# Performance work log

Measured on AMD Instinct MI355X. Metric: run time of the kernel, lower is better.

The kernel has to match this reference:

```python
import jax, jax.numpy as jnp
import numpy as np

N = 50000
E = 800000
DES, TW, NUMP, CATP = 768, 768, 4, 3
EMB = 384
THIRD = EMB // 3  # 128


def _lin(key, fan_in, fan_out):
    k1, k2 = jax.random.split(key)
    bound = 1.0 / np.sqrt(fan_in)
    W = jax.random.uniform(k1, (fan_in, fan_out), jnp.float32, -bound, bound)
    b = jax.random.uniform(k2, (fan_out,), jnp.float32, -bound, bound)
    return W, b


def setup_inputs() -> dict:
    key = jax.random.key(0)
    ks = jax.random.split(key, 16)
    des = jax.random.normal(ks[0], (N, DES), jnp.float32)
    tweet = jax.random.normal(ks[1], (N, TW), jnp.float32)
    num_prop = jax.random.normal(ks[2], (N, NUMP), jnp.float32)
    cat_prop = jax.random.normal(ks[3], (N, CATP), jnp.float32)
    edge_index = jax.random.randint(ks[4], (2, E), 0, N, jnp.int64)
    W_des, b_des = _lin(ks[5], DES, THIRD)
    W_num, b_num = _lin(ks[6], NUMP, THIRD)
    W_cat, b_cat = _lin(ks[7], CATP, THIRD)
    W_in, b_in = _lin(ks[8], EMB, EMB)
    W_g1, b_g1 = _lin(ks[9], EMB, EMB)
    W_g2, b_g2 = _lin(ks[10], EMB, EMB)
    W_o1, b_o1 = _lin(ks[11], EMB, EMB)
    W_o2, b_o2 = _lin(ks[12], EMB, 2)
    return dict(des=des, tweet=tweet, num_prop=num_prop, cat_prop=cat_prop,
                edge_index=edge_index,
                W_des=W_des, b_des=b_des, W_num=W_num, b_num=b_num,
                W_cat=W_cat, b_cat=b_cat, W_in=W_in, b_in=b_in,
                W_g1=W_g1, b_g1=b_g1, W_g2=W_g2, b_g2=b_g2,
                W_o1=W_o1, b_o1=b_o1, W_o2=W_o2, b_o2=b_o2)


def _leaky(x):
    return jax.nn.leaky_relu(x, 0.01)


def _gcn_conv(x, edge_index, W, b):
    # PyG GCNConv: x' = D^{-1/2} (A + I) D^{-1/2} (x W) + b
    src, dst = edge_index[0], edge_index[1]
    x = x @ W  # [N, out]
    n = x.shape[0]
    deg = jax.ops.segment_sum(jnp.ones(src.shape[0], x.dtype), dst, num_segments=n) + 1.0  # self-loop
    dinv = jax.lax.rsqrt(deg)  # deg >= 1
    norm = dinv[src] * dinv[dst]  # [E]
    msg = x[src] * norm[:, None]  # [E, out] gather
    agg = jax.ops.segment_sum(msg, dst, num_segments=n)  # scatter-add
    agg = agg + x * (dinv * dinv)[:, None]  # self-loop contribution
    return agg + b


def reference(des, tweet, num_prop, cat_prop, edge_index,
              W_des, b_des, W_num, b_num, W_cat, b_cat, W_in, b_in,
              W_g1, b_g1, W_g2, b_g2, W_o1, b_o1, W_o2, b_o2):
    # eval mode: dropout is identity
    d = _leaky(des @ W_des + b_des)
    n = _leaky(num_prop @ W_num + b_num)
    c = _leaky(cat_prop @ W_cat + b_cat)
    x = jnp.concatenate((d, n, c), axis=1)  # [N, EMB]
    x = _leaky(x @ W_in + b_in)
    x = _gcn_conv(x, edge_index, W_g1, b_g1)
    x = _gcn_conv(x, edge_index, W_g2, b_g2)
    x = _leaky(x @ W_o1 + b_o1)
    return x @ W_o2 + b_o2  # [N, 2]
```

## Files before the change

### kernel.cpp

```cpp
#include <hip/hip_runtime.h>
#include <hip/hip_bf16.h>
#include <cstdint>

#define NFEAT 384
#define DESK 768
#define THIRD 128

typedef __bf16 bf16x8 __attribute__((ext_vector_type(8)));
typedef unsigned short u16x8 __attribute__((ext_vector_type(8)));
typedef unsigned short u16x4 __attribute__((ext_vector_type(4)));
typedef float f32x16 __attribute__((ext_vector_type(16)));
typedef _Float16 h16x2 __attribute__((ext_vector_type(2)));

__device__ __forceinline__ float leaky(float x) { return x > 0.f ? x : 0.01f * x; }

__device__ __forceinline__ unsigned short bfhi(float x) {
  unsigned int u = __float_as_uint(x);
  u += 0x7fffu + ((u >> 16) & 1u);
  return (unsigned short)(u >> 16);
}
__device__ __forceinline__ float bf2f(unsigned short h) {
  return __uint_as_float(((unsigned int)h) << 16);
}
__device__ __forceinline__ void bsplit(float x, unsigned short& h,
                                       unsigned short& l) {
  h = bfhi(x);
  l = bfhi(x - bf2f(h));
}

__device__ __forceinline__ int swz(int kb, int row, int ROWS) {
  return (kb * ROWS + (row ^ (kb << 1))) * 8;
}

#define MFMA(a, b, c) __builtin_amdgcn_mfma_f32_32x32x16_bf16(a, b, c, 0, 0, 0)

template <int AFP32, int EPI, int BM, int DBUF>
__global__ __launch_bounds__(256, 2) void mfma_gemm(
    const float* __restrict__ Af, const unsigned short* __restrict__ Ahi,
    const unsigned short* __restrict__ Alo,
    const unsigned short* __restrict__ BThi,
    const unsigned short* __restrict__ BTlo, _Float16* __restrict__ Ch16,
    unsigned short* __restrict__ Chi, unsigned short* __restrict__ Clo,
    const float* __restrict__ bias, int M, int K, int ldc) {
  __shared__ unsigned short AhiL[DBUF + 1][4 * BM * 8];
  __shared__ unsigned short AloL[DBUF + 1][4 * BM * 8];
  __shared__ unsigned short BhiL[DBUF + 1][4 * 128 * 8];
  __shared__ unsigned short BloL[DBUF + 1][4 * 128 * 8];
  const int tid = threadIdx.x;
  const int lane = tid & 63;
  const int w = tid >> 6;
  constexpr int MR = BM / 64;
  const int wm = (w >> 1) * (BM / 2);
  const int wn = (w & 1) * 64;
  const int lm = lane & 31, lk = lane >> 5;

  int bx = blockIdx.x, by = blockIdx.y;
  if (gridDim.y == 3) {
    int lin = by * gridDim.x + bx;
    int ng = gridDim.x >> 3;
    int full = ng * 24;
    if (lin < full) {
      int g = lin / 24, x = lin - g * 24;
      bx = g * 8 + (x & 7);
      by = x >> 3;
    } else {
      int rem = lin - full;
      int mrem = gridDim.x - (ng << 3);
      bx = (ng << 3) + rem % mrem;
      by = rem / mrem;
    }
  }
  const int m_base = bx * BM, n_base = by * 128;

  f32x16 acc[MR][2];
#pragma unroll
  for (int mi = 0; mi < MR; mi++)
#pragma unroll
    for (int nt = 0; nt < 2; nt++)
#pragma unroll
      for (int r = 0; r < 16; r++) acc[mi][nt][r] = 0.f;

  constexpr int AIT_F = BM / 32;
  constexpr int AIT_H = BM / 64;
  float4 pa[3][AIT_F];
  u16x8 pah[3][AIT_H], pal[3][AIT_H];
  u16x8 pbh[3][2], pbl[3][2];

  auto loadA = [&](int kt, int s) {
    if (AFP32) {
#pragma unroll
      for (int it = 0; it < AIT_F; it++) {
        int r = (tid >> 3) + it * 32;
        int gr = m_base + r;
        float4 av = make_float4(0.f, 0.f, 0.f, 0.f);
        if (gr < M) av = *(const float4*)&Af[(size_t)gr * K + kt + (tid & 7) * 4];
        pa[s][it] = av;
      }
    } else {
#pragma unroll
      for (int it = 0; it < AIT_H; it++) {
        int r = (tid >> 2) + it * 64;
        int gr = m_base + r;
        u16x8 vh = {0, 0, 0, 0, 0, 0, 0, 0};
        u16x8 vl = {0, 0, 0, 0, 0, 0, 0, 0};
        if (gr < M) {
          vh = *(const u16x8*)&Ahi[(size_t)gr * K + kt + (tid & 3) * 8];
          vl = *(const u16x8*)&Alo[(size_t)gr * K + kt + (tid & 3) * 8];
        }
        pah[s][it] = vh;
        pal[s][it] = vl;
      }
    }
  };
  auto loadB = [&](int kt, int s) {
#pragma unroll
    for (int it = 0; it < 2; it++) {
      int n = (tid >> 2) + it * 64;
      pbh[s][it] = *(const u16x8*)&BThi[(size_t)(n_base + n) * K + kt + (tid & 3) * 8];
      pbl[s][it] = *(const u16x8*)&BTlo[(size_t)(n_base + n) * K + kt + (tid & 3) * 8];
    }
  };
  auto storeLDS = [&](int s, int b) {
    if (AFP32) {
#pragma unroll
      for (int it = 0; it < AIT_F; it++) {
        int r = (tid >> 3) + it * 32;
        int q = tid & 7;
        float4 av = pa[s][it];
        unsigned short h0, h1, h2, h3, l0, l1, l2, l3;
        bsplit(av.x, h0, l0);
        bsplit(av.y, h1, l1);
        bsplit(av.z, h2, l2);
        bsplit(av.w, h3, l3);
        int base = swz(q >> 1, r, BM) + (q & 1) * 4;
        u16x4 th;
        th.x = h0; th.y = h1; th.z = h2; th.w = h3;
        u16x4 tl;
        tl.x = l0; tl.y = l1; tl.z = l2; tl.w = l3;
        *(u16x4*)&AhiL[b][base] = th;
        *(u16x4*)&AloL[b][base] = tl;
      }
    } else {
#pragma unroll
      for (int it = 0; it < AIT_H; it++) {
        int r = (tid >> 2) + it * 64;
        int kb = tid & 3;
        *(u16x8*)&AhiL[b][swz(kb, r, BM)] = pah[s][it];
        *(u16x8*)&AloL[b][swz(kb, r, BM)] = pal[s][it];
      }
    }
#pragma unroll
    for (int it = 0; it < 2; it++) {
      int n = (tid >> 2) + it * 64;
      int kb = tid & 3;
      *(u16x8*)&BhiL[b][swz(kb, n, 128)] = pbh[s][it];
      *(u16x8*)&BloL[b][swz(kb, n, 128)] = pbl[s][it];
    }
  };
  auto compute = [&](int b) {
#pragma unroll
    for (int ks = 0; ks < 2; ks++) {
      int kb = 2 * ks + lk;
      bf16x8 ah[MR], al[MR];
#pragma unroll
      for (int mi = 0; mi < MR; mi++) {
        ah[mi] = __builtin_bit_cast(
            bf16x8, *(const u16x8*)&AhiL[b][swz(kb, wm + mi * 32 + lm, BM)]);
        al[mi] = __builtin_bit_cast(
            bf16x8, *(const u16x8*)&AloL[b][swz(kb, wm + mi * 32 + lm, BM)]);
      }
      bf16x8 bh0 = __builtin_bit_cast(
          bf16x8, *(const u16x8*)&BhiL[b][swz(kb, wn + lm, 128)]);
      bf16x8 bh1 = __builtin_bit_cast(
          bf16x8, *(const u16x8*)&BhiL[b][swz(kb, wn + 32 + lm, 128)]);
      bf16x8 bl0 = __builtin_bit_cast(
          bf16x8, *(const u16x8*)&BloL[b][swz(kb, wn + lm, 128)]);
      bf16x8 bl1 = __builtin_bit_cast(
          bf16x8, *(const u16x8*)&BloL[b][swz(kb, wn + 32 + lm, 128)]);
#pragma unroll
      for (int mi = 0; mi < MR; mi++) {
        acc[mi][0] = MFMA(ah[mi], bh0, acc[mi][0]);
        acc[mi][1] = MFMA(ah[mi], bh1, acc[mi][1]);
        acc[mi][0] = MFMA(ah[mi], bl0, acc[mi][0]);
        acc[mi][1] = MFMA(ah[mi], bl1, acc[mi][1]);
        acc[mi][0] = MFMA(al[mi], bh0, acc[mi][0]);
        acc[mi][1] = MFMA(al[mi], bh1, acc[mi][1]);
      }
    }
  };

  const int NK = K >> 5;
  loadA(0, 0);
  loadB(0, 0);
  loadA(32, 1);
  loadB(32, 1);
  loadA(64, 2);
  loadB(64, 2);

  if (DBUF) {
    storeLDS(0, 0);
    __syncthreads();
    for (int m6 = 0; m6 < NK / 6; m6++) {
#pragma unroll
      for (int ph = 0; ph < 6; ph++) {
        const int i = m6 * 6 + ph;
        if (i + 1 < NK) storeLDS((ph + 1) % 3, (ph + 1) & 1);
        if (i + 3 < NK) {
          loadA((i + 3) << 5, ph % 3);
          loadB((i + 3) << 5, ph % 3);
        }
        compute(ph & 1);
        __syncthreads();
      }
    }
  } else {
    for (int m3 = 0; m3 < NK / 3; m3++) {
#pragma unroll
      for (int ph = 0; ph < 3; ph++) {
        const int i = m3 * 3 + ph;
        storeLDS(ph, 0);
        __syncthreads();
        if (i + 3 < NK) {
          loadA((i + 3) << 5, ph);
          loadB((i + 3) << 5, ph);
        }
        compute(0);
        __syncthreads();
      }
    }
  }

  const int colb = n_base + wn;
#pragma unroll
  for (int mi = 0; mi < MR; mi++) {
#pragma unroll
    for (int nt = 0; nt < 2; nt++) {
      f32x16 v = acc[mi][nt];
      int col = colb + nt * 32 + lm;
      float bv = (EPI == 0) ? bias[col] : 0.f;
      int rb = m_base + wm + mi * 32 + 4 * lk;
      int p = col / 48;
      size_t pbase = (size_t)p * M * 48 + (col - p * 48);
#pragma unroll
      for (int rg = 0; rg < 16; rg++) {
        int row = rb + (rg & 3) + 8 * (rg >> 2);
        if (row < M) {
          float x = v[rg];
          if (EPI == 0) {
            x = leaky(x + bv);
            unsigned short h, l;
            bsplit(x, h, l);
            Chi[(size_t)row * ldc + col] = h;
            Clo[(size_t)row * ldc + col] = l;
          } else {
            Ch16[pbase + (size_t)row * 48] = (_Float16)x;
          }
        }
      }
    }
  }
}

__global__ __launch_bounds__(256) void split_transpose_b(
    const float* __restrict__ s0, unsigned short* __restrict__ h0,
    unsigned short* __restrict__ l0, const float* __restrict__ s1,
    unsigned short* __restrict__ h1, unsigned short* __restrict__ l1,
    const float* __restrict__ s2, unsigned short* __restrict__ h2,
    unsigned short* __restrict__ l2) {
  int z = blockIdx.z;
  const float* src = z == 0 ? s0 : (z == 1 ? s1 : s2);
  unsigned short* dsthi = z == 0 ? h0 : (z == 1 ? h1 : h2);
  unsigned short* dstlo = z == 0 ? l0 : (z == 1 ? l1 : l2);
  int R = z == 0 ? 768 : 384;
  int C = z == 0 ? 128 : 384;
  int c0 = blockIdx.x * 32, r0 = blockIdx.y * 32;
  if (c0 >= C || r0 >= R) return;
  __shared__ float tile[32][33];
  int tx = threadIdx.x & 31, ty = threadIdx.x >> 5;
#pragma unroll
  for (int i = 0; i < 4; i++)
    tile[ty + i * 8][tx] = src[(size_t)(r0 + ty + i * 8) * C + c0 + tx];
  __syncthreads();
#pragma unroll
  for (int i = 0; i < 4; i++) {
    int c = c0 + ty + i * 8, r = r0 + tx;
    float v = tile[tx][ty + i * 8];
    unsigned short h, l;
    bsplit(v, h, l);
    dsthi[(size_t)c * R + r] = h;
    dstlo[(size_t)c * R + r] = l;
  }
}

__global__ __launch_bounds__(256) void gemm384(const float* __restrict__ A,
                                               const float* __restrict__ B,
                                               float* __restrict__ C) {
  __shared__ float As[16][68];
  __shared__ float Bs[16][64];
  const int tid = threadIdx.x;
  const int mb = blockIdx.x * 64;
  const int nb = blockIdx.y * 64;
  float acc[4][4] = {};
  const int arow = tid >> 2, akq = tid & 3;
  const int brow = tid >> 4, bc4 = tid & 15;
  const int m0 = (tid >> 4) * 4, n0 = (tid & 15) * 4;
  for (int kk = 0; kk < 384; kk += 16) {
    float4 av = *(const float4*)&A[(mb + arow) * 384 + kk + akq * 4];
    As[akq * 4 + 0][arow] = av.x;
    As[akq * 4 + 1][arow] = av.y;
    As[akq * 4 + 2][arow] = av.z;
    As[akq * 4 + 3][arow] = av.w;
    *(float4*)&Bs[brow][bc4 * 4] =
        *(const float4*)&B[(kk + brow) * 384 + nb + bc4 * 4];
    __syncthreads();
#pragma unroll
    for (int k = 0; k < 16; k++) {
      float4 a4 = *(const float4*)&As[k][m0];
      float4 b4 = *(const float4*)&Bs[k][n0];
      float a[4] = {a4.x, a4.y, a4.z, a4.w};
      float b[4] = {b4.x, b4.y, b4.z, b4.w};
#pragma unroll
      for (int i = 0; i < 4; i++)
#pragma unroll
        for (int j = 0; j < 4; j++) acc[i][j] = fmaf(a[i], b[j], acc[i][j]);
    }
    __syncthreads();
  }
#pragma unroll
  for (int i = 0; i < 4; i++)
#pragma unroll
    for (int j = 0; j < 4; j++)
      C[(mb + m0 + i) * 384 + nb + n0 + j] = acc[i][j];
}

__global__ void uv_kernel(const float* __restrict__ T1,
                          const float* __restrict__ W_o1,
                          const float* __restrict__ b_g1,
                          const float* __restrict__ b_g2,
                          const float* __restrict__ b_o1, float* __restrict__ u,
                          float* __restrict__ v) {
  int j = blockIdx.x * blockDim.x + threadIdx.x;
  if (j < 384) {
    float su = 0.f, sv = 0.f;
    for (int k = 0; k < 384; k++) {
      su = fmaf(T1[k * 384 + j], b_g1[k], su);
      sv = fmaf(W_o1[k * 384 + j], b_g2[k], sv);
    }
    u[j] = su;
    v[j] = sv + b_o1[j];
  }
}

__global__ __launch_bounds__(256) void numcat_kernel(
    const float* __restrict__ num, const float* __restrict__ cat,
    const float* __restrict__ Wn, const float* __restrict__ bn,
    const float* __restrict__ Wc, const float* __restrict__ bc,
    unsigned short* __restrict__ x0hi, unsigned short* __restrict__ x0lo,
    int N) {
  int c = threadIdx.x;
  for (int i = blockIdx.x; i < N; i += gridDim.x) {
    float val;
    if (c < 128) {
      val = bn[c];
      val = fmaf(num[i * 4 + 0], Wn[0 * 128 + c], val);
      val = fmaf(num[i * 4 + 1], Wn[1 * 128 + c], val);
      val = fmaf(num[i * 4 + 2], Wn[2 * 128 + c], val);
      val = fmaf(num[i * 4 + 3], Wn[3 * 128 + c], val);
    } else {
      int cc = c - 128;
      val = bc[cc];
      val = fmaf(cat[i * 3 + 0], Wc[0 * 128 + cc], val);
      val = fmaf(cat[i * 3 + 1], Wc[1 * 128 + cc], val);
      val = fmaf(cat[i * 3 + 2], Wc[2 * 128 + cc], val);
    }
    val = leaky(val);
    unsigned short h, l;
    bsplit(val, h, l);
    size_t o = (size_t)i * NFEAT + 128 + c;
    x0hi[o] = h;
    x0lo[o] = l;
  }
}

__global__ void count_kernel(const int* __restrict__ dst, int* __restrict__ deg,
                             int E) {
  int e = blockIdx.x * blockDim.x + threadIdx.x;
  if (e < E) atomicAdd(&deg[dst[e]], 1);
}

__global__ void scan_reduce(const int* __restrict__ deg,
                            int* __restrict__ partial, int N) {
  __shared__ int sm[512];
  int i = blockIdx.x * 512 + threadIdx.x;
  sm[threadIdx.x] = (i < N) ? deg[i] : 0;
  __syncthreads();
  for (int off = 256; off; off >>= 1) {
    if (threadIdx.x < off) sm[threadIdx.x] += sm[threadIdx.x + off];
    __syncthreads();
  }
  if (threadIdx.x == 0) partial[blockIdx.x] = sm[0];
}

__global__ void scan_top(int* partial, int nb) {
  if (threadIdx.x == 0 && blockIdx.x == 0) {
    int run = 0;
    for (int b = 0; b < nb; b++) {
      int t = partial[b];
      partial[b] = run;
      run += t;
    }
  }
}

__global__ void scan_down(const int* __restrict__ deg,
                          const int* __restrict__ partial,
                          int* __restrict__ offsets, int* __restrict__ cursor,
                          float* __restrict__ dinv, int N, int E) {
  __shared__ int sm[512];
  int t = threadIdx.x;
  int i = blockIdx.x * 512 + t;
  int val = (i < N) ? deg[i] : 0;
  sm[t] = val;
  __syncthreads();
  for (int off = 1; off < 512; off <<= 1) {
    int add = (t >= off) ? sm[t - off] : 0;
    __syncthreads();
    sm[t] += add;
    __syncthreads();
  }
  if (i < N) {
    int ex = partial[blockIdx.x] + sm[t] - val;
    offsets[i] = ex;
    cursor[i] = ex;
    dinv[i] = 1.0f / sqrtf((float)val + 1.0f);
  }
  if (i == 0) offsets[N] = E;
}

__global__ void fill_kernel(const int* __restrict__ src,
                            const int* __restrict__ dst,
                            int* __restrict__ cursor,
                            int* __restrict__ csr_off,
                            float* __restrict__ csr_w,
                            const float* __restrict__ dinv, int E) {
  int e = blockIdx.x * blockDim.x + threadIdx.x;
  if (e < E) {
    int s = src[e], d = dst[e];
    int slot = atomicAdd(&cursor[d], 1);
    csr_off[slot] = s * 48;
    csr_w[slot] = dinv[s] * dinv[d];
  }
}

__global__ void init_out(const float* __restrict__ b_o2,
                         float* __restrict__ out, int N) {
  int i = blockIdx.x * blockDim.x + threadIdx.x;
  if (i < N) {
    out[2 * i + 0] = b_o2[0];
    out[2 * i + 1] = b_o2[1];
  }
}

template <int WRITE_S, int FINAL>
__global__ __launch_bounds__(192) void agg_slice(
    const _Float16* __restrict__ xin, _Float16* __restrict__ xout,
    const int* __restrict__ offsets, const int* __restrict__ csr_off,
    const float* __restrict__ csr_w, const float* __restrict__ dinv,
    float* __restrict__ sout, const float* __restrict__ svec,
    const float* __restrict__ uvec, const float* __restrict__ vvec,
    const float* __restrict__ W_o2, float* __restrict__ out, int N) {
  const int t = threadIdx.x;
  const int team = t / 24;
  const int l = t - team * 24;
  const int slice = blockIdx.x & 7;
  const int sb = blockIdx.x >> 3;
  const int teams_per_slice = (gridDim.x >> 3) * 8;
  const _Float16* xp = xin + (size_t)slice * N * 48;
  const int t0 = sb * 8 + team;
  __shared__ float red[192][2];

  float u0 = 0.f, u1 = 0.f, vc0 = 0.f, vc1 = 0.f;
  float w00 = 0.f, w01 = 0.f, w10 = 0.f, w11 = 0.f;
  if (FINAL) {
    const int f = slice * 48 + 2 * l;
    u0 = uvec[f];
    u1 = uvec[f + 1];
    vc0 = vvec[f];
    vc1 = vvec[f + 1];
    w00 = W_o2[f * 2 + 0];
    w01 = W_o2[f * 2 + 1];
    w10 = W_o2[(f + 1) * 2 + 0];
    w11 = W_o2[(f + 1) * 2 + 1];
  }

  auto dorow = [&](int i, float& ax, float& ay, float& wsum) {
    int beg = offsets[i], end = offsets[i + 1];
    float di = dinv[i];
    float dii = di * di;
    h16x2 xs = *(const h16x2*)&xp[(size_t)i * 48 + 2 * l];
    float A0x = dii * (float)xs.x, A0y = dii * (float)xs.y;
    float A1x = 0.f, A1y = 0.f, A2x = 0.f, A2y = 0.f, A3x = 0.f, A3y = 0.f;
    wsum = dii;
    int j = beg;
    for (; j + 8 <= end; j += 8) {
      int o0 = csr_off[j + 0], o1 = csr_off[j + 1], o2 = csr_off[j + 2],
          o3 = csr_off[j + 3];
      int o4 = csr_off[j + 4], o5 = csr_off[j + 5], o6 = csr_off[j + 6],
          o7 = csr_off[j + 7];
      float w0 = csr_w[j + 0], w1 = csr_w[j + 1], w2 = csr_w[j + 2],
            w3 = csr_w[j + 3];
      float w4 = csr_w[j + 4], w5 = csr_w[j + 5], w6 = csr_w[j + 6],
            w7 = csr_w[j + 7];
      h16x2 v0 = *(const h16x2*)&xp[o0 + 2 * l];
      h16x2 v1 = *(const h16x2*)&xp[o1 + 2 * l];
      h16x2 v2 = *(const h16x2*)&xp[o2 + 2 * l];
      h16x2 v3 = *(const h16x2*)&xp[o3 + 2 * l];
      h16x2 v4 = *(const h16x2*)&xp[o4 + 2 * l];
      h16x2 v5 = *(const h16x2*)&xp[o5 + 2 * l];
      h16x2 v6 = *(const h16x2*)&xp[o6 + 2 * l];
      h16x2 v7 = *(const h16x2*)&xp[o7 + 2 * l];
      A0x = fmaf(w0, (float)v0.x, A0x);
      A0y = fmaf(w0, (float)v0.y, A0y);
      A1x = fmaf(w1, (float)v1.x, A1x);
      A1y = fmaf(w1, (float)v1.y, A1y);
      A2x = fmaf(w2, (float)v2.x, A2x);
      A2y = fmaf(w2, (float)v2.y, A2y);
      A3x = fmaf(w3, (float)v3.x, A3x);
      A3y = fmaf(w3, (float)v3.y, A3y);
      A0x = fmaf(w4, (float)v4.x, A0x);
      A0y = fmaf(w4, (float)v4.y, A0y);
      A1x = fmaf(w5, (float)v5.x, A1x);
      A1y = fmaf(w5, (float)v5.y, A1y);
      A2x = fmaf(w6, (float)v6.x, A2x);
      A2y = fmaf(w6, (float)v6.y, A2y);
      A3x = fmaf(w7, (float)v7.x, A3x);
      A3y = fmaf(w7, (float)v7.y, A3y);
      if (WRITE_S) wsum += ((w0 + w1) + (w2 + w3)) + ((w4 + w5) + (w6 + w7));
    }
    for (; j < end; j++) {
      float wj = csr_w[j];
      h16x2 vj = *(const h16x2*)&xp[csr_off[j] + 2 * l];
      A0x = fmaf(wj, (float)vj.x, A0x);
      A0y = fmaf(wj, (float)vj.y, A0y);
      if (WRITE_S) wsum += wj;
    }
    ax = (A0x + A1x) + (A2x + A3x);
    ay = (A0y + A1y) + (A2y + A3y);
  };

  if (FINAL) {
    const int iters = (N + teams_per_slice - 1) / teams_per_slice;
    for (int it = 0; it < iters; it++) {
      const int i = t0 + it * teams_per_slice;
      float c0 = 0.f, c1 = 0.f;
      if (i < N) {
        float ax, ay, wsum;
        dorow(i, ax, ay, wsum);
        float si = svec[i];
        float q0 = leaky(ax + si * u0 + vc0);
        float q1 = leaky(ay + si * u1 + vc1);
        c0 = q0 * w00 + q1 * w10;
        c1 = q0 * w01 + q1 * w11;
      }
      red[t][0] = c0;
      red[t][1] = c1;
      __syncthreads();
      if (t < 16) {
        int tm = t >> 1, c = t & 1;
        int i2 = sb * 8 + tm + it * teams_per_slice;
        if (i2 < N) {
          float s = 0.f;
#pragma unroll
          for (int k = 0; k < 24; k++) s += red[tm * 24 + k][c];
          atomicAdd(&out[i2 * 2 + c], s);
        }
      }
      __syncthreads();
    }
  } else {
    _Float16* op = xout + (size_t)slice * N * 48;
    for (int i = t0; i < N; i += teams_per_slice) {
      float ax, ay, wsum;
      dorow(i, ax, ay, wsum);
      h16x2 r;
      r.x = (_Float16)ax;
      r.y = (_Float16)ay;
      *(h16x2*)&op[(size_t)i * 48 + 2 * l] = r;
      if (WRITE_S && slice == 0 && l == 0) sout[i] = wsum;
    }
  }
}

extern "C" void kernel_launch(void* const* d_in, const int* in_sizes, int n_in,
                              void* d_out, int out_size, void* d_ws,
                              size_t ws_size, hipStream_t stream) {
  const float* des = (const float*)d_in[0];
  const float* num_prop = (const float*)d_in[2];
  const float* cat_prop = (const float*)d_in[3];
  const int* edge = (const int*)d_in[4];
  const float* W_des = (const float*)d_in[5];
  const float* b_des = (const float*)d_in[6];
  const float* W_num = (const float*)d_in[7];
  const float* b_num = (const float*)d_in[8];
  const float* W_cat = (const float*)d_in[9];
  const float* b_cat = (const float*)d_in[10];
  const float* W_in = (const float*)d_in[11];
  const float* b_in = (const float*)d_in[12];
  const float* W_g1 = (const float*)d_in[13];
  const float* b_g1 = (const float*)d_in[14];
  const float* W_g2 = (const float*)d_in[15];
  const float* b_g2 = (const float*)d_in[16];
  const float* W_o1 = (const float*)d_in[17];
  const float* b_o1 = (const float*)d_in[18];
  const float* W_o2 = (const float*)d_in[19];
  const float* b_o2 = (const float*)d_in[20];
  float* out = (float*)d_out;

  const int N = in_sizes[0] / DESK;
  const int E = in_sizes[4] / 2;
  const int* esrc = edge;
  const int* edst = edge + E;

  char* ws = (char*)d_ws;
  size_t off = 0;
  auto alloc = [&](size_t n) {
    off = (off + 255) & ~(size_t)255;
    size_t o = off;
    off += n;
    return o;
  };
  float* bufA = (float*)(ws + alloc((size_t)N * NFEAT * 4));
  float* bufB = (float*)(ws + alloc((size_t)N * NFEAT * 4));
  int* deg = (int*)(ws + alloc((size_t)N * 4));
  int* offsets = (int*)(ws + alloc((size_t)(N + 1) * 4));
  int* cursor = (int*)(ws + alloc((size_t)N * 4));
  int* partial = (int*)(ws + alloc(1024 * 4));
  float* dinv = (float*)(ws + alloc((size_t)N * 4));
  float* svec = (float*)(ws + alloc((size_t)N * 4));
  int* csr_off = (int*)(ws + alloc((size_t)E * 4));
  float* csr_w = (float*)(ws + alloc((size_t)E * 4));
  float* T1 = (float*)(ws + alloc(384 * 384 * 4));
  float* Mmat = (float*)(ws + alloc(384 * 384 * 4));
  float* uvec = (float*)(ws + alloc(384 * 4));
  float* vvec = (float*)(ws + alloc(384 * 4));
  unsigned short* WdThi = (unsigned short*)(ws + alloc(768 * 128 * 2));
  unsigned short* WdTlo = (unsigned short*)(ws + alloc(768 * 128 * 2));
  unsigned short* WiThi = (unsigned short*)(ws + alloc(384 * 384 * 2));
  unsigned short* WiTlo = (unsigned short*)(ws + alloc(384 * 384 * 2));
  unsigned short* MmThi = (unsigned short*)(ws + alloc(384 * 384 * 2));
  unsigned short* MmTlo = (unsigned short*)(ws + alloc(384 * 384 * 2));
  (void)ws_size;
  (void)n_in;
  (void)out_size;

  unsigned short* x0hi = (unsigned short*)bufA;
  unsigned short* x0lo = x0hi + (size_t)N * NFEAT;
  unsigned short* x1hi = (unsigned short*)bufB;
  unsigned short* x1lo = x1hi + (size_t)N * NFEAT;
  _Float16* yb = (_Float16*)bufA;
  _Float16* w1 = (_Float16*)bufB;

  hipMemsetAsync(deg, 0, (size_t)N * 4, stream);

  dim3 g6(6, 6);
  gemm384<<<g6, 256, 0, stream>>>(W_g2, W_o1, T1);
  gemm384<<<g6, 256, 0, stream>>>(W_g1, T1, Mmat);
  uv_kernel<<<2, 256, 0, stream>>>(T1, W_o1, b_g1, b_g2, b_o1, uvec, vvec);
  split_transpose_b<<<dim3(12, 24, 3), 256, 0, stream>>>(
      W_des, WdThi, WdTlo, W_in, WiThi, WiTlo, Mmat, MmThi, MmTlo);

  const int MT = (N + 127) / 128;
  const int MT64 = (N + 63) / 64;
  mfma_gemm<1, 0, 64, 0><<<dim3(MT64, 1), 256, 0, stream>>>(
      des, nullptr, nullptr, WdThi, WdTlo, nullptr, x0hi, x0lo, b_des, N, DESK,
      NFEAT);
  numcat_kernel<<<1024, 256, 0, stream>>>(num_prop, cat_prop, W_num, b_num,
                                          W_cat, b_cat, x0hi, x0lo, N);
  mfma_gemm<0, 0, 128, 1><<<dim3(MT, 3), 256, 0, stream>>>(
      nullptr, x0hi, x0lo, WiThi, WiTlo, nullptr, x1hi, x1lo, b_in, N, NFEAT,
      NFEAT);
  mfma_gemm<0, 1, 128, 1><<<dim3(MT, 3), 256, 0, stream>>>(
      nullptr, x1hi, x1lo, MmThi, MmTlo, yb, nullptr, nullptr, nullptr, N,
      NFEAT, NFEAT);

  const int EB = (E + 255) / 256;
  count_kernel<<<EB, 256, 0, stream>>>(edst, deg, E);
  const int NB = (N + 511) / 512;
  scan_reduce<<<NB, 512, 0, stream>>>(deg, partial, N);
  scan_top<<<1, 64, 0, stream>>>(partial, NB);
  scan_down<<<NB, 512, 0, stream>>>(deg, partial, offsets, cursor, dinv, N, E);
  fill_kernel<<<EB, 256, 0, stream>>>(esrc, edst, cursor, csr_off, csr_w, dinv,
                                      E);
  init_out<<<(N + 255) / 256, 256, 0, stream>>>(b_o2, out, N);

  const int NBS = 512;
  agg_slice<1, 0><<<8 * NBS, 192, 0, stream>>>(
      yb, w1, offsets, csr_off, csr_w, dinv, svec, nullptr, nullptr, nullptr,
      nullptr, nullptr, N);
  agg_slice<0, 1><<<8 * NBS, 192, 0, stream>>>(
      w1, nullptr, offsets, csr_off, csr_w, dinv, nullptr, svec, uvec, vvec,
      W_o2, out, N);
}
```

Measured before the change: 1.023 ms.

## Parallelize GCN aggregation across edges within a block instead of rows per team

Result: slower. 1.453 ms (+42.1%).

```diff
diff --git a/kernel.cpp b/kernel.cpp
--- a/kernel.cpp
+++ b/kernel.cpp
@@ -462,7 +462,7 @@
 }
 
 template <int WRITE_S, int FINAL>
-__global__ __launch_bounds__(192) void agg_slice(
+__global__ __launch_bounds__(192) void agg_ep(
     const _Float16* __restrict__ xin, _Float16* __restrict__ xout,
     const int* __restrict__ offsets, const int* __restrict__ csr_off,
     const float* __restrict__ csr_w, const float* __restrict__ dinv,
@@ -470,19 +470,23 @@
     const float* __restrict__ uvec, const float* __restrict__ vvec,
     const float* __restrict__ W_o2, float* __restrict__ out, int N) {
   const int t = threadIdx.x;
-  const int team = t / 24;
-  const int l = t - team * 24;
+  const int e8 = t / 24;
+  const int l = t - e8 * 24;
   const int slice = blockIdx.x & 7;
   const int sb = blockIdx.x >> 3;
-  const int teams_per_slice = (gridDim.x >> 3) * 8;
+  const int nsb = gridDim.x >> 3;
   const _Float16* xp = xin + (size_t)slice * N * 48;
-  const int t0 = sb * 8 + team;
-  __shared__ float red[192][2];
+  _Float16* op = FINAL ? nullptr : xout + (size_t)slice * N * 48;
+  __shared__ int ssrc[64];
+  __shared__ float sw[64];
+  __shared__ float red[8][24][2];
+  __shared__ float rw[8];
+  __shared__ float rc[24][2];
 
   float u0 = 0.f, u1 = 0.f, vc0 = 0.f, vc1 = 0.f;
   float w00 = 0.f, w01 = 0.f, w10 = 0.f, w11 = 0.f;
-  if (FINAL) {
-    const int f = slice * 48 + 2 * l;
+  if (FINAL && t < 24) {
+    const int f = slice * 48 + 2 * t;
     u0 = uvec[f];
     u1 = uvec[f + 1];
     vc0 = vvec[f];
@@ -493,100 +497,74 @@
     w11 = W_o2[(f + 1) * 2 + 1];
   }
 
-  auto dorow = [&](int i, float& ax, float& ay, float& wsum) {
-    int beg = offsets[i], end = offsets[i + 1];
-    float di = dinv[i];
-    float dii = di * di;
-    h16x2 xs = *(const h16x2*)&xp[(size_t)i * 48 + 2 * l];
-    float A0x = dii * (float)xs.x, A0y = dii * (float)xs.y;
-    float A1x = 0.f, A1y = 0.f, A2x = 0.f, A2y = 0.f, A3x = 0.f, A3y = 0.f;
-    wsum = dii;
-    int j = beg;
-    for (; j + 8 <= end; j += 8) {
-      int o0 = csr_off[j + 0], o1 = csr_off[j + 1], o2 = csr_off[j + 2],
-          o3 = csr_off[j + 3];
-      int o4 = csr_off[j + 4], o5 = csr_off[j + 5], o6 = csr_off[j + 6],
-          o7 = csr_off[j + 7];
-      float w0 = csr_w[j + 0], w1 = csr_w[j + 1], w2 = csr_w[j + 2],
-            w3 = csr_w[j + 3];
-      float w4 = csr_w[j + 4], w5 = csr_w[j + 5], w6 = csr_w[j + 6],
-            w7 = csr_w[j + 7];
-      h16x2 v0 = *(const h16x2*)&xp[o0 + 2 * l];
-      h16x2 v1 = *(const h16x2*)&xp[o1 + 2 * l];
-      h16x2 v2 = *(const h16x2*)&xp[o2 + 2 * l];
-      h16x2 v3 = *(const h16x2*)&xp[o3 + 2 * l];
-      h16x2 v4 = *(const h16x2*)&xp[o4 + 2 * l];
-      h16x2 v5 = *(const h16x2*)&xp[o5 + 2 * l];
-      h16x2 v6 = *(const h16x2*)&xp[o6 + 2 * l];
-      h16x2 v7 = *(const h16x2*)&xp[o7 + 2 * l];
-      A0x = fmaf(w0, (float)v0.x, A0x);
-      A0y = fmaf(w0, (float)v0.y, A0y);
-      A1x = fmaf(w1, (float)v1.x, A1x);
-      A1y = fmaf(w1, (float)v1.y, A1y);
-      A2x = fmaf(w2, (float)v2.x, A2x);
-      A2y = fmaf(w2, (float)v2.y, A2y);
-      A3x = fmaf(w3, (float)v3.x, A3x);
-      A3y = fmaf(w3, (float)v3.y, A3y);
-      A0x = fmaf(w4, (float)v4.x, A0x);
-      A0y = fmaf(w4, (float)v4.y, A0y);
-      A1x = fmaf(w5, (float)v5.x, A1x);
-      A1y = fmaf(w5, (float)v5.y, A1y);
-      A2x = fmaf(w6, (float)v6.x, A2x);
-      A2y = fmaf(w6, (float)v6.y, A2y);
-      A3x = fmaf(w7, (float)v7.x, A3x);
-      A3y = fmaf(w7, (float)v7.y, A3y);
-      if (WRITE_S) wsum += ((w0 + w1) + (w2 + w3)) + ((w4 + w5) + (w6 + w7));
-    }
-    for (; j < end; j++) {
-      float wj = csr_w[j];
-      h16x2 vj = *(const h16x2*)&xp[csr_off[j] + 2 * l];
-      A0x = fmaf(wj, (float)vj.x, A0x);
-      A0y = fmaf(wj, (float)vj.y, A0y);
-      if (WRITE_S) wsum += wj;
-    }
-    ax = (A0x + A1x) + (A2x + A3x);
-    ay = (A0y + A1y) + (A2y + A3y);
-  };
-
-  if (FINAL) {
-    const int iters = (N + teams_per_slice - 1) / teams_per_slice;
-    for (int it = 0; it < iters; it++) {
-      const int i = t0 + it * teams_per_slice;
-      float c0 = 0.f, c1 = 0.f;
-      if (i < N) {
-        float ax, ay, wsum;
-        dorow(i, ax, ay, wsum);
+  for (int i = sb; i < N; i += nsb) {
+    const int beg = offsets[i];
+    const int deg = offsets[i + 1] - beg;
+    float ax = 0.f, ay = 0.f, wp = 0.f;
+    for (int j0 = 0; j0 < deg; j0 += 64) {
+      int cnt = min(64, deg - j0);
+      int cntp = (cnt + 7) & ~7;
+      if (t < 64) {
+        if (t < cnt) {
+          ssrc[t] = csr_off[beg + j0 + t];
+          sw[t] = csr_w[beg + j0 + t];
+        } else {
+          ssrc[t] = 0;
+          sw[t] = 0.f;
+        }
+      }
+      __syncthreads();
+      for (int j = e8; j < cntp; j += 8) {
+        float wj = sw[j];
+        h16x2 vj = *(const h16x2*)&xp[ssrc[j] + 2 * l];
+        ax = fmaf(wj, (float)vj.x, ax);
+        ay = fmaf(wj, (float)vj.y, ay);
+        if (WRITE_S) wp += wj;
+      }
+      __syncthreads();
+    }
+    red[e8][l][0] = ax;
+    red[e8][l][1] = ay;
+    if (WRITE_S && l == 0) rw[e8] = wp;
+    __syncthreads();
+    if (t < 24) {
+      float di = dinv[i];
+      float dii = di * di;
+      h16x2 xs = *(const h16x2*)&xp[(size_t)i * 48 + 2 * t];
+      float sx = dii * (float)xs.x, sy = dii * (float)xs.y;
+#pragma unroll
+      for (int k = 0; k < 8; k++) {
+        sx += red[k][t][0];
+        sy += red[k][t][1];
+      }
+      if (!FINAL) {
+        h16x2 r;
+        r.x = (_Float16)sx;
+        r.y = (_Float16)sy;
+        *(h16x2*)&op[(size_t)i * 48 + 2 * t] = r;
+        if (WRITE_S && slice == 0 && t == 0) {
+          float wsum = dii;
+#pragma unroll
+          for (int k = 0; k < 8; k++) wsum += rw[k];
+          sout[i] = wsum;
+        }
+      } else {
         float si = svec[i];
-        float q0 = leaky(ax + si * u0 + vc0);
-        float q1 = leaky(ay + si * u1 + vc1);
-        c0 = q0 * w00 + q1 * w10;
-        c1 = q0 * w01 + q1 * w11;
-      }
-      red[t][0] = c0;
-      red[t][1] = c1;
+        float q0 = leaky(sx + si * u0 + vc0);
+        float q1 = leaky(sy + si * u1 + vc1);
+        rc[t][0] = q0 * w00 + q1 * w10;
+        rc[t][1] = q0 * w01 + q1 * w11;
+      }
+    }
+    if (FINAL) {
       __syncthreads();
-      if (t < 16) {
-        int tm = t >> 1, c = t & 1;
-        int i2 = sb * 8 + tm + it * teams_per_slice;
-        if (i2 < N) {
-          float s = 0.f;
-#pragma unroll
-          for (int k = 0; k < 24; k++) s += red[tm * 24 + k][c];
-          atomicAdd(&out[i2 * 2 + c], s);
-        }
+      if (t < 2) {
+        float s = 0.f;
+#pragma unroll
+        for (int k = 0; k < 24; k++) s += rc[k][t];
+        atomicAdd(&out[i * 2 + t], s);
       }
       __syncthreads();
-    }
-  } else {
-    _Float16* op = xout + (size_t)slice * N * 48;
-    for (int i = t0; i < N; i += teams_per_slice) {
-      float ax, ay, wsum;
-      dorow(i, ax, ay, wsum);
-      h16x2 r;
-      r.x = (_Float16)ax;
-      r.y = (_Float16)ay;
-      *(h16x2*)&op[(size_t)i * 48 + 2 * l] = r;
-      if (WRITE_S && slice == 0 && l == 0) sout[i] = wsum;
     }
   }
 }
@@ -694,10 +672,10 @@
   init_out<<<(N + 255) / 256, 256, 0, stream>>>(b_o2, out, N);
 
   const int NBS = 512;
-  agg_slice<1, 0><<<8 * NBS, 192, 0, stream>>>(
+  agg_ep<1, 0><<<8 * NBS, 192, 0, stream>>>(
       yb, w1, offsets, csr_off, csr_w, dinv, svec, nullptr, nullptr, nullptr,
       nullptr, nullptr, N);
-  agg_slice<0, 1><<<8 * NBS, 192, 0, stream>>>(
+  agg_ep<0, 1><<<8 * NBS, 192, 0, stream>>>(
       w1, nullptr, offsets, csr_off, csr_w, dinv, nullptr, svec, uvec, vvec,
       W_o2, out, N);
 }
```
